# Kernel tuning notes

Hardware: AMD Instinct MI355X
Metric: run time of the kernel (lower is better)

Reference implementation:

```python
import jax, jax.numpy as jnp
import numpy as np

ITERS = 3
K = 64
C = 256


def setup_inputs() -> dict:
    key = jax.random.key(0)
    ks = jax.random.split(key, 6)
    N, H, W = 2, 60, 60
    cnn_feature = jax.random.normal(ks[0], (N, C, H, W), dtype=jnp.float32)
    points = jax.random.normal(ks[1], (N, 3, H, W), dtype=jnp.float32)
    # torch Linear params: weight (out, in), bias (out,)
    s1 = 1.0 / np.sqrt(C)
    s2 = 1.0 / np.sqrt(2 * C)
    mlp_w = jax.random.uniform(ks[2], (C, C), jnp.float32, -s1, s1)
    mlp_b = jax.random.uniform(ks[3], (C,), jnp.float32, -s1, s1)
    rnn_w = jax.random.uniform(ks[4], (C, 2 * C), jnp.float32, -s2, s2)
    rnn_b = jax.random.uniform(ks[5], (C,), jnp.float32, -s2, s2)
    return {"cnn_feature": cnn_feature, "points": points, "mlp_w": mlp_w,
            "mlp_b": mlp_b, "rnn_w": rnn_w, "rnn_b": rnn_b}


def reference(cnn_feature, points, mlp_w, mlp_b, rnn_w, rnn_b):
    N, Cc, H, W = cnn_feature.shape
    HW = H * W
    pts = points.reshape(N, 3, HW).transpose(0, 2, 1)  # (N, HW, 3)
    # pairwise Euclidean distances via Gram matrix
    r = jnp.einsum('nid,njd->nij', pts, pts)           # (N, HW, HW)
    sq = jnp.einsum('nid,nid->ni', pts, pts)           # (N, HW)
    D = jnp.sqrt(jnp.maximum(sq[:, :, None] + sq[:, None, :] - 2.0 * r, 0.0))
    _, idx = jax.lax.top_k(-D, K)                      # (N, HW, K) smallest distances

    h = cnn_feature.transpose(0, 2, 3, 1).reshape(N, HW, Cc)  # (N, HW, C)
    bidx = jnp.arange(N)[:, None, None]
    for _ in range(ITERS):
        nb = h[bidx, idx]                              # (N, HW, K, C) gather
        nb = jax.nn.relu(jnp.einsum('nskc,dc->nskd', nb, mlp_w) + mlp_b)
        message = nb.mean(axis=2)                      # (N, HW, C)
        nh = jnp.concatenate([h, message], axis=-1)    # (N, HW, 2C)
        h = jax.nn.relu(jnp.einsum('nsc,dc->nsd', nh, rnn_w) + rnn_b)
    h = h.reshape(N, H, W, Cc).transpose(0, 3, 1, 2)   # (N, C, H, W)
    return jnp.concatenate([cnn_feature, h], axis=1)   # (N, 2C, H, W)
```

## Files before the change

### kernel.cpp

```cpp
#include <hip/hip_runtime.h>
#include <stdint.h>

typedef unsigned int uint;

#define HW 3600
#define NBATCH 2
#define CDIM 256
#define KNN 64
#define M_REAL 7200
#define PADM 7232
#define QPB 8

using short8  = __attribute__((ext_vector_type(8))) short;
using floatx4 = __attribute__((ext_vector_type(4))) float;

__device__ inline unsigned short f2bf(float f) {
    uint u = __float_as_uint(f);
    uint r = u + 0x7FFFu + ((u >> 16) & 1u);
    return (unsigned short)(r >> 16);
}
__device__ inline float bf2f(unsigned short b) {
    return __uint_as_float(((uint)b) << 16);
}

__device__ inline void wave_select(uint* hist, uint* s_bin, uint* s_want,
                                   int lane, uint want) {
    uint h0 = hist[4 * lane + 0], h1 = hist[4 * lane + 1];
    uint h2 = hist[4 * lane + 2], h3 = hist[4 * lane + 3];
    hist[4 * lane + 0] = 0; hist[4 * lane + 1] = 0;
    hist[4 * lane + 2] = 0; hist[4 * lane + 3] = 0;
    uint c4 = h0 + h1 + h2 + h3;
    uint v = c4;
    #pragma unroll
    for (int off = 1; off < 64; off <<= 1) {
        uint o = __shfl_up(v, off, 64);
        if (lane >= off) v += o;
    }
    uint below = v - c4;
    if (below < want && want <= v) {
        uint b = 4 * lane, c = below;
        if (c + h0 < want) { c += h0; b = 4 * lane + 1;
            if (c + h1 < want) { c += h1; b = 4 * lane + 2;
                if (c + h2 < want) { c += h2; b = 4 * lane + 3; } } }
        *s_bin = b;
        *s_want = want - c;
    }
}

__global__ __launch_bounds__(512) void topk_kernel(const float* __restrict__ points,
                                                   int* __restrict__ idx_out) {
    const int wv = threadIdx.x >> 6;
    const int lane = threadIdx.x & 63;
    const int q = blockIdx.x * QPB + wv;
    const int n = (blockIdx.x * QPB) / HW;
    const int i = q - n * HW;

    __shared__ __align__(16) float sx[HW], sy[HW], sz[HW];
    __shared__ uint hist[QPB][256];
    __shared__ uint s_bin[QPB], s_want[QPB], s_cnt[QPB];

    const float* __restrict__ px = points + (size_t)n * 3 * HW;

    for (int j4 = threadIdx.x; j4 < HW / 4; j4 += 512) {
        *(float4*)&sx[j4 * 4] = ((const float4*)px)[j4];
        *(float4*)&sy[j4 * 4] = ((const float4*)px)[j4 + HW / 4];
        *(float4*)&sz[j4 * 4] = ((const float4*)px)[j4 + 2 * (HW / 4)];
    }
    hist[wv][4 * lane + 0] = 0; hist[wv][4 * lane + 1] = 0;
    hist[wv][4 * lane + 2] = 0; hist[wv][4 * lane + 3] = 0;
    if (lane == 0) s_cnt[wv] = 0;
    __syncthreads();

    const float xi = sx[i], yi = sy[i], zi = sz[i];
    const float sqi = xi * xi + yi * yi + zi * zi;

    uint qp[30];
    #pragma unroll
    for (int c = 0; c < 30; ++c) qp[c] = 0xFFFFFFFFu;
    #pragma unroll
    for (int c = 0; c < 15; ++c) {
        int j0 = (c << 8) + lane * 4;
        if (j0 < HW) {
            float4 x4 = *(const float4*)&sx[j0];
            float4 y4 = *(const float4*)&sy[j0];
            float4 z4 = *(const float4*)&sz[j0];
            float d0 = fmaxf(sqi + (x4.x * x4.x + y4.x * y4.x + z4.x * z4.x)
                             - 2.0f * (xi * x4.x + yi * y4.x + zi * z4.x), 0.0f);
            float d1 = fmaxf(sqi + (x4.y * x4.y + y4.y * y4.y + z4.y * z4.y)
                             - 2.0f * (xi * x4.y + yi * y4.y + zi * z4.y), 0.0f);
            float d2 = fmaxf(sqi + (x4.z * x4.z + y4.z * y4.z + z4.z * z4.z)
                             - 2.0f * (xi * x4.z + yi * y4.z + zi * z4.z), 0.0f);
            float d3 = fmaxf(sqi + (x4.w * x4.w + y4.w * y4.w + z4.w * z4.w)
                             - 2.0f * (xi * x4.w + yi * y4.w + zi * z4.w), 0.0f);
            uint k0 = (uint)fminf(d0 * 1024.0f, 65535.0f);
            uint k1 = (uint)fminf(d1 * 1024.0f, 65535.0f);
            uint k2 = (uint)fminf(d2 * 1024.0f, 65535.0f);
            uint k3 = (uint)fminf(d3 * 1024.0f, 65535.0f);
            qp[2 * c]     = k0 | (k1 << 16);
            qp[2 * c + 1] = k2 | (k3 << 16);
        }
    }
    #define Q16(c, t) ((qp[2 * (c) + ((t) >> 1)] >> (((t) & 1) << 4)) & 0xFFFFu)

    #pragma unroll
    for (int c = 0; c < 15; ++c)
        #pragma unroll
        for (int t = 0; t < 4; ++t) atomicAdd(&hist[wv][Q16(c, t) >> 8], 1u);
    __syncthreads();
    wave_select(&hist[wv][0], &s_bin[wv], &s_want[wv], lane, KNN);
    __syncthreads();
    const uint qT8 = s_bin[wv];
    const uint want2 = s_want[wv];
    __syncthreads();

    #pragma unroll
    for (int c = 0; c < 15; ++c)
        #pragma unroll
        for (int t = 0; t < 4; ++t) {
            uint k = Q16(c, t);
            if ((k >> 8) == qT8) atomicAdd(&hist[wv][k & 255u], 1u);
        }
    __syncthreads();
    wave_select(&hist[wv][0], &s_bin[wv], &s_want[wv], lane, want2);
    __syncthreads();
    const uint qT16 = (qT8 << 8) | s_bin[wv];
    const uint want3 = s_want[wv];

    #pragma unroll
    for (int c = 0; c < 15; ++c)
        #pragma unroll
        for (int t = 0; t < 4; ++t) {
            if (Q16(c, t) < qT16) {
                uint pos = atomicAdd(&s_cnt[wv], 1u);
                if (pos < KNN)
                    idx_out[(size_t)q * KNN + pos] = (c << 8) + lane * 4 + t;
            }
        }
    unsigned long long used = 0ULL;
    const int base = KNN - (int)want3;
    for (int r = 0; r < (int)want3; ++r) {
        unsigned long long best = ~0ULL;
        #pragma unroll
        for (int c = 0; c < 15; ++c) {
            int j0 = (c << 8) + lane * 4;
            if (j0 < HW) {
                float4 x4 = *(const float4*)&sx[j0];
                float4 y4 = *(const float4*)&sy[j0];
                float4 z4 = *(const float4*)&sz[j0];
                float dd[4];
                dd[0] = fmaxf(sqi + (x4.x * x4.x + y4.x * y4.x + z4.x * z4.x)
                              - 2.0f * (xi * x4.x + yi * y4.x + zi * z4.x), 0.0f);
                dd[1] = fmaxf(sqi + (x4.y * x4.y + y4.y * y4.y + z4.y * z4.y)
                              - 2.0f * (xi * x4.y + yi * y4.y + zi * z4.y), 0.0f);
                dd[2] = fmaxf(sqi + (x4.z * x4.z + y4.z * y4.z + z4.z * z4.z)
                              - 2.0f * (xi * x4.z + yi * y4.z + zi * z4.z), 0.0f);
                dd[3] = fmaxf(sqi + (x4.w * x4.w + y4.w * y4.w + z4.w * z4.w)
                              - 2.0f * (xi * x4.w + yi * y4.w + zi * z4.w), 0.0f);
                #pragma unroll
                for (int t = 0; t < 4; ++t) {
                    int slot = c * 4 + t;
                    if (Q16(c, t) == qT16 && !((used >> slot) & 1ULL)) {
                        unsigned long long key =
                            ((unsigned long long)__float_as_uint(dd[t]) << 32)
                            | (uint)(j0 + t);
                        if (key < best) best = key;
                    }
                }
            }
        }
        #pragma unroll
        for (int off = 1; off < 64; off <<= 1) {
            unsigned long long o = __shfl_xor(best, off, 64);
            if (o < best) best = o;
        }
        uint jw = (uint)best;
        if (lane == 0) idx_out[(size_t)q * KNN + base + r] = (int)jw;
        if ((int)((jw & 255u) >> 2) == lane)
            used |= 1ULL << (((jw >> 8) << 2) | (jw & 3u));
    }
    #undef Q16
}

__global__ __launch_bounds__(256) void setup_kernel(
    const float* __restrict__ mw, const float* __restrict__ rw,
    unsigned short* __restrict__ mo, unsigned short* __restrict__ ro) {
    int i = blockIdx.x * 256 + threadIdx.x;
    if (i < 65536) mo[i] = f2bf(mw[i]);
    ro[i] = f2bf(rw[i]);
}

__global__ __launch_bounds__(256) void init_h(const float* __restrict__ cnn,
                                              unsigned short* __restrict__ NH,
                                              float* __restrict__ out) {
    __shared__ float tile[32][33];
    const int hw0 = blockIdx.x * 32;
    const int c0 = blockIdx.y * 32;
    const int n = blockIdx.z;
    const int tx = threadIdx.x & 31;
    const int ty = threadIdx.x >> 5;
    const float* __restrict__ src = cnn + (size_t)n * CDIM * HW;
    #pragma unroll
    for (int r = 0; r < 4; ++r) {
        int cc = ty + r * 8;
        int hw = hw0 + tx;
        if (hw < HW) {
            float v = src[(size_t)(c0 + cc) * HW + hw];
            tile[cc][tx] = v;
            out[(size_t)n * (2 * CDIM * HW) + (size_t)(c0 + cc) * HW + hw] = v;
        }
    }
    __syncthreads();
    #pragma unroll
    for (int r = 0; r < 4; ++r) {
        int hh = ty + r * 8;
        int hw = hw0 + hh;
        if (hw < HW) NH[(size_t)(n * HW + hw) * 512 + c0 + tx] = f2bf(tile[tx][hh]);
    }
}

#define LDKP 264
__global__ __launch_bounds__(256) void gemm_mfma(
    const unsigned short* __restrict__ A, int lda,
    const unsigned short* __restrict__ W, int ldw,
    const float* __restrict__ bias,
    unsigned short* __restrict__ Cb, int ldc,
    float* __restrict__ outp, int mode, int Kk) {
    __shared__ __align__(16) unsigned short As[64 * LDKP];
    __shared__ __align__(16) unsigned short Bs[64 * LDKP];
    const int m0 = blockIdx.x * 64;
    const int n0 = blockIdx.y * 64;
    const int tid = threadIdx.x;
    const int lane = tid & 63;
    const int w = tid >> 6;
    const int wm = (w & 1) * 32;
    const int wn = (w >> 1) * 32;
    const int l15 = lane & 15;
    const int qd = lane >> 4;

    floatx4 acc[2][2];
    #pragma unroll
    for (int a = 0; a < 2; ++a)
        #pragma unroll
        for (int b = 0; b < 2; ++b)
            acc[a][b] = (floatx4){0.f, 0.f, 0.f, 0.f};

    const int srow = tid >> 5;
    const int scol = (tid & 31) * 8;

    for (int k0 = 0; k0 < Kk; k0 += 256) {
        if (k0) __syncthreads();
        #pragma unroll
        for (int r8 = 0; r8 < 8; ++r8) {
            int row = r8 * 8 + srow;
            *(float4*)&As[row * LDKP + scol] =
                *(const float4*)&A[(size_t)(m0 + row) * lda + k0 + scol];
            *(float4*)&Bs[row * LDKP + scol] =
                *(const float4*)&W[(size_t)(n0 + row) * ldw + k0 + scol];
        }
        __syncthreads();
        #pragma unroll
        for (int ks = 0; ks < 256; ks += 32) {
            short8 a0 = *(const short8*)&As[(wm + l15) * LDKP + ks + qd * 8];
            short8 a1 = *(const short8*)&As[(wm + 16 + l15) * LDKP + ks + qd * 8];
            short8 b0 = *(const short8*)&Bs[(wn + l15) * LDKP + ks + qd * 8];
            short8 b1 = *(const short8*)&Bs[(wn + 16 + l15) * LDKP + ks + qd * 8];
            acc[0][0] = __builtin_amdgcn_mfma_f32_16x16x32_bf16(a0, b0, acc[0][0], 0, 0, 0);
            acc[0][1] = __builtin_amdgcn_mfma_f32_16x16x32_bf16(a0, b1, acc[0][1], 0, 0, 0);
            acc[1][0] = __builtin_amdgcn_mfma_f32_16x16x32_bf16(a1, b0, acc[1][0], 0, 0, 0);
            acc[1][1] = __builtin_amdgcn_mfma_f32_16x16x32_bf16(a1, b1, acc[1][1], 0, 0, 0);
        }
    }

    #pragma unroll
    for (int in = 0; in < 2; ++in) {
        int col = n0 + wn + in * 16 + l15;
        float bv = bias[col];
        #pragma unroll
        for (int im = 0; im < 2; ++im) {
            int mb = m0 + wm + im * 16 + qd * 4;
            if (mode == 0) {
                #pragma unroll
                for (int r = 0; r < 4; ++r)
                    Cb[(size_t)(mb + r) * ldc + col] =
                        f2bf(fmaxf(acc[im][in][r] + bv, 0.0f));
            } else if (mb < M_REAL) {
                int nb = mb / HW;
                int hw = mb - nb * HW;
                float4 o;
                o.x = fmaxf(acc[im][in][0] + bv, 0.0f);
                o.y = fmaxf(acc[im][in][1] + bv, 0.0f);
                o.z = fmaxf(acc[im][in][2] + bv, 0.0f);
                o.w = fmaxf(acc[im][in][3] + bv, 0.0f);
                *(float4*)&outp[(size_t)nb * (2 * CDIM * HW)
                                + (size_t)(CDIM + col) * HW + hw] = o;
            }
        }
    }
}

__global__ __launch_bounds__(256) void gather_mean(const unsigned short* __restrict__ T,
                                                   const int* __restrict__ idx,
                                                   unsigned short* __restrict__ NH) {
    const int q = blockIdx.x * 4 + (threadIdx.x >> 6);
    const int lane = threadIdx.x & 63;
    const int n = q / HW;
    const int half = lane >> 5;
    const int c8 = (lane & 31) * 8;

    const int nbrL = idx[(size_t)q * KNN + lane];
    float acc[8] = {0, 0, 0, 0, 0, 0, 0, 0};
    #pragma unroll 4
    for (int it = 0; it < 32; ++it) {
        int k = 2 * it + half;
        int j = __shfl(nbrL, k, 64);
        j = min(max(j, 0), HW - 1);
        int r = n * HW + j;
        uint4 v = *(const uint4*)&T[(size_t)r * CDIM + c8];
        acc[0] += bf2f((unsigned short)(v.x & 0xFFFFu));
        acc[1] += bf2f((unsigned short)(v.x >> 16));
        acc[2] += bf2f((unsigned short)(v.y & 0xFFFFu));
        acc[3] += bf2f((unsigned short)(v.y >> 16));
        acc[4] += bf2f((unsigned short)(v.z & 0xFFFFu));
        acc[5] += bf2f((unsigned short)(v.z >> 16));
        acc[6] += bf2f((unsigned short)(v.w & 0xFFFFu));
        acc[7] += bf2f((unsigned short)(v.w >> 16));
    }
    #pragma unroll
    for (int c = 0; c < 8; ++c) acc[c] += __shfl_xor(acc[c], 32, 64);
    if (half == 0) {
        uint4 o;
        o.x = (uint)f2bf(acc[0] * (1.0f / KNN)) | ((uint)f2bf(acc[1] * (1.0f / KNN)) << 16);
        o.y = (uint)f2bf(acc[2] * (1.0f / KNN)) | ((uint)f2bf(acc[3] * (1.0f / KNN)) << 16);
        o.z = (uint)f2bf(acc[4] * (1.0f / KNN)) | ((uint)f2bf(acc[5] * (1.0f / KNN)) << 16);
        o.w = (uint)f2bf(acc[6] * (1.0f / KNN)) | ((uint)f2bf(acc[7] * (1.0f / KNN)) << 16);
        *(uint4*)&NH[(size_t)q * 512 + CDIM + c8] = o;
    }
}

extern "C" void kernel_launch(void* const* d_in, const int* in_sizes, int n_in,
                              void* d_out, int out_size, void* d_ws, size_t ws_size,
                              hipStream_t stream) {
    const float* cnn   = (const float*)d_in[0];
    const float* pts   = (const float*)d_in[1];
    const float* mlp_w = (const float*)d_in[2];
    const float* mlp_b = (const float*)d_in[3];
    const float* rnn_w = (const float*)d_in[4];
    const float* rnn_b = (const float*)d_in[5];
    float* out = (float*)d_out;

    unsigned short* NHa    = (unsigned short*)d_ws;
    unsigned short* NHb    = NHa + (size_t)PADM * 512;
    unsigned short* Tb     = NHb + (size_t)PADM * 512;
    unsigned short* mlpw_b = Tb + (size_t)PADM * CDIM;
    unsigned short* rnnw_b = mlpw_b + 65536;
    int*            idx    = (int*)(rnnw_b + 131072);

    setup_kernel<<<512, 256, 0, stream>>>(mlp_w, rnn_w, mlpw_b, rnnw_b);
    topk_kernel<<<M_REAL / QPB, 512, 0, stream>>>(pts, idx);
    init_h<<<dim3(113, 8, NBATCH), 256, 0, stream>>>(cnn, NHa, out);

    unsigned short* cur = NHa;
    unsigned short* nxt = NHb;
    for (int it = 0; it < 3; ++it) {
        gemm_mfma<<<dim3(PADM / 64, CDIM / 64), 256, 0, stream>>>(
            cur, 512, mlpw_b, CDIM, mlp_b, Tb, CDIM, nullptr, 0, CDIM);
        gather_mean<<<M_REAL / 4, 256, 0, stream>>>(Tb, idx, cur);
        if (it < 2) {
            gemm_mfma<<<dim3(PADM / 64, CDIM / 64), 256, 0, stream>>>(
                cur, 512, rnnw_b, 512, rnn_b, nxt, 512, nullptr, 0, 512);
            unsigned short* tmp = cur; cur = nxt; nxt = tmp;
        } else {
            gemm_mfma<<<dim3(PADM / 64, CDIM / 64), 256, 0, stream>>>(
                cur, 512, rnnw_b, 512, rnn_b, nullptr, 0, out, 1, 512);
        }
    }
}
```

Before: 243.3 us.

## Merge setup, top-k and init kernels into one launch; cache tie-bin candidates

The three independent prologue kernels (bf16 weight conversion, kNN top-k selection, feature transpose/init) become one heterogeneous kernel dispatched by block index, so they share a single launch and can run concurrently on the device. The top-k path changes its point layout to interleaved float4 with a strided per-lane assignment, and for the final tie bin it caches up to four candidate keys per lane in registers instead of recomputing all distances each selection round. A fallback keeps the old rescan loop when any lane holds more than four tie candidates. The shared-memory union sizes every block for the top-k footprint, which may limit occupancy of the lighter block types.

After: 206.9 us. 15.0% less time.

```diff
diff --git a/kernel.cpp b/kernel.cpp
--- a/kernel.cpp
+++ b/kernel.cpp
@@ -2,6 +2,7 @@
 #include <stdint.h>
 
 typedef unsigned int uint;
+typedef unsigned long long ull;
 
 #define HW 3600
 #define NBATCH 2
@@ -10,6 +11,10 @@
 #define M_REAL 7200
 #define PADM 7232
 #define QPB 8
+
+#define TKB 900
+#define IHB 904
+#define SUB 64
 
 using short8  = __attribute__((ext_vector_type(8))) short;
 using floatx4 = __attribute__((ext_vector_type(4))) float;
@@ -47,175 +52,200 @@
     }
 }
 
-__global__ __launch_bounds__(512) void topk_kernel(const float* __restrict__ points,
-                                                   int* __restrict__ idx_out) {
+union MegaSmem {
+    struct {
+        float4 pts[HW];
+        uint hist[QPB][256];
+        uint s_bin[QPB], s_want[QPB], s_cnt[QPB];
+    } tk;
+    struct { float tile[2][32][33]; } ih;
+};
+
+__global__ __launch_bounds__(512) void mega_kernel(
+    const float* __restrict__ points, int* __restrict__ idx_out,
+    const float* __restrict__ cnn, unsigned short* __restrict__ NH,
+    float* __restrict__ out,
+    const float* __restrict__ mw, const float* __restrict__ rw,
+    unsigned short* __restrict__ mo, unsigned short* __restrict__ ro) {
+    __shared__ MegaSmem sm;
+    const int blk = blockIdx.x;
+
+    if (blk >= TKB + IHB) {
+        int i0 = (blk - TKB - IHB) * 2048 + threadIdx.x * 4;
+        float4 v = *(const float4*)&rw[i0];
+        uint2 p;
+        p.x = (uint)f2bf(v.x) | ((uint)f2bf(v.y) << 16);
+        p.y = (uint)f2bf(v.z) | ((uint)f2bf(v.w) << 16);
+        *(uint2*)&ro[i0] = p;
+        if (i0 < 65536) {
+            float4 m = *(const float4*)&mw[i0];
+            p.x = (uint)f2bf(m.x) | ((uint)f2bf(m.y) << 16);
+            p.y = (uint)f2bf(m.z) | ((uint)f2bf(m.w) << 16);
+            *(uint2*)&mo[i0] = p;
+        }
+        return;
+    }
+
+    if (blk >= TKB) {
+        const int b = blk - TKB;
+        const int n = b / 452;
+        const int r = b - n * 452;
+        const int hw0 = (r % 113) * 32;
+        const int c0 = (r / 113) * 64 + ((threadIdx.x >> 8) << 5);
+        const int t8 = threadIdx.x & 255;
+        const int tx = t8 & 31;
+        const int ty = t8 >> 5;
+        float (*tile)[33] = sm.ih.tile[threadIdx.x >> 8];
+        const float* __restrict__ src = cnn + (size_t)n * CDIM * HW;
+        #pragma unroll
+        for (int rr = 0; rr < 4; ++rr) {
+            int cc = ty + rr * 8;
+            int hw = hw0 + tx;
+            if (hw < HW) {
+                float v = src[(size_t)(c0 + cc) * HW + hw];
+                tile[cc][tx] = v;
+                out[(size_t)n * (2 * CDIM * HW) + (size_t)(c0 + cc) * HW + hw] = v;
+            }
+        }
+        __syncthreads();
+        #pragma unroll
+        for (int rr = 0; rr < 4; ++rr) {
+            int hh = ty + rr * 8;
+            int hw = hw0 + hh;
+            if (hw < HW)
+                NH[(size_t)(n * HW + hw) * 512 + c0 + tx] = f2bf(tile[tx][hh]);
+        }
+        return;
+    }
+
     const int wv = threadIdx.x >> 6;
     const int lane = threadIdx.x & 63;
-    const int q = blockIdx.x * QPB + wv;
-    const int n = (blockIdx.x * QPB) / HW;
+    const int q = blk * QPB + wv;
+    const int n = (blk * QPB) / HW;
     const int i = q - n * HW;
 
-    __shared__ __align__(16) float sx[HW], sy[HW], sz[HW];
-    __shared__ uint hist[QPB][256];
-    __shared__ uint s_bin[QPB], s_want[QPB], s_cnt[QPB];
-
     const float* __restrict__ px = points + (size_t)n * 3 * HW;
-
-    for (int j4 = threadIdx.x; j4 < HW / 4; j4 += 512) {
-        *(float4*)&sx[j4 * 4] = ((const float4*)px)[j4];
-        *(float4*)&sy[j4 * 4] = ((const float4*)px)[j4 + HW / 4];
-        *(float4*)&sz[j4 * 4] = ((const float4*)px)[j4 + 2 * (HW / 4)];
-    }
-    hist[wv][4 * lane + 0] = 0; hist[wv][4 * lane + 1] = 0;
-    hist[wv][4 * lane + 2] = 0; hist[wv][4 * lane + 3] = 0;
-    if (lane == 0) s_cnt[wv] = 0;
-    __syncthreads();
-
-    const float xi = sx[i], yi = sy[i], zi = sz[i];
+    const float* __restrict__ py = px + HW;
+    const float* __restrict__ pz = py + HW;
+
+    for (int j = threadIdx.x; j < HW; j += 512)
+        sm.tk.pts[j] = make_float4(px[j], py[j], pz[j], 0.0f);
+    sm.tk.hist[wv][4 * lane + 0] = 0; sm.tk.hist[wv][4 * lane + 1] = 0;
+    sm.tk.hist[wv][4 * lane + 2] = 0; sm.tk.hist[wv][4 * lane + 3] = 0;
+    if (lane == 0) sm.tk.s_cnt[wv] = 0;
+    __syncthreads();
+
+    float4 pq = sm.tk.pts[i];
+    const float xi = pq.x, yi = pq.y, zi = pq.z;
     const float sqi = xi * xi + yi * yi + zi * zi;
 
-    uint qp[30];
-    #pragma unroll
-    for (int c = 0; c < 30; ++c) qp[c] = 0xFFFFFFFFu;
-    #pragma unroll
-    for (int c = 0; c < 15; ++c) {
-        int j0 = (c << 8) + lane * 4;
-        if (j0 < HW) {
-            float4 x4 = *(const float4*)&sx[j0];
-            float4 y4 = *(const float4*)&sy[j0];
-            float4 z4 = *(const float4*)&sz[j0];
-            float d0 = fmaxf(sqi + (x4.x * x4.x + y4.x * y4.x + z4.x * z4.x)
-                             - 2.0f * (xi * x4.x + yi * y4.x + zi * z4.x), 0.0f);
-            float d1 = fmaxf(sqi + (x4.y * x4.y + y4.y * y4.y + z4.y * z4.y)
-                             - 2.0f * (xi * x4.y + yi * y4.y + zi * z4.y), 0.0f);
-            float d2 = fmaxf(sqi + (x4.z * x4.z + y4.z * y4.z + z4.z * z4.z)
-                             - 2.0f * (xi * x4.z + yi * y4.z + zi * z4.z), 0.0f);
-            float d3 = fmaxf(sqi + (x4.w * x4.w + y4.w * y4.w + z4.w * z4.w)
-                             - 2.0f * (xi * x4.w + yi * y4.w + zi * z4.w), 0.0f);
-            uint k0 = (uint)fminf(d0 * 1024.0f, 65535.0f);
-            uint k1 = (uint)fminf(d1 * 1024.0f, 65535.0f);
-            uint k2 = (uint)fminf(d2 * 1024.0f, 65535.0f);
-            uint k3 = (uint)fminf(d3 * 1024.0f, 65535.0f);
-            qp[2 * c]     = k0 | (k1 << 16);
-            qp[2 * c + 1] = k2 | (k3 << 16);
-        }
-    }
-    #define Q16(c, t) ((qp[2 * (c) + ((t) >> 1)] >> (((t) & 1) << 4)) & 0xFFFFu)
-
-    #pragma unroll
-    for (int c = 0; c < 15; ++c)
-        #pragma unroll
-        for (int t = 0; t < 4; ++t) atomicAdd(&hist[wv][Q16(c, t) >> 8], 1u);
-    __syncthreads();
-    wave_select(&hist[wv][0], &s_bin[wv], &s_want[wv], lane, KNN);
-    __syncthreads();
-    const uint qT8 = s_bin[wv];
-    const uint want2 = s_want[wv];
-    __syncthreads();
-
-    #pragma unroll
-    for (int c = 0; c < 15; ++c)
-        #pragma unroll
-        for (int t = 0; t < 4; ++t) {
-            uint k = Q16(c, t);
-            if ((k >> 8) == qT8) atomicAdd(&hist[wv][k & 255u], 1u);
-        }
-    __syncthreads();
-    wave_select(&hist[wv][0], &s_bin[wv], &s_want[wv], lane, want2);
-    __syncthreads();
-    const uint qT16 = (qT8 << 8) | s_bin[wv];
-    const uint want3 = s_want[wv];
-
-    #pragma unroll
-    for (int c = 0; c < 15; ++c)
-        #pragma unroll
-        for (int t = 0; t < 4; ++t) {
-            if (Q16(c, t) < qT16) {
-                uint pos = atomicAdd(&s_cnt[wv], 1u);
-                if (pos < KNN)
-                    idx_out[(size_t)q * KNN + pos] = (c << 8) + lane * 4 + t;
+    uint qp[29];
+    #pragma unroll
+    for (int s = 0; s < 57; ++s) {
+        int j = (s << 6) + lane;
+        uint q16 = 0xFFFFu;
+        if (j < HW) {
+            float4 p = sm.tk.pts[j];
+            float d2 = fmaxf(sqi + (p.x * p.x + p.y * p.y + p.z * p.z)
+                             - 2.0f * (xi * p.x + yi * p.y + zi * p.z), 0.0f);
+            q16 = (uint)fminf(d2 * 1024.0f, 65535.0f);
+        }
+        if (s & 1) qp[s >> 1] |= q16 << 16; else qp[s >> 1] = q16;
+    }
+    #define Q16(s) ((qp[(s) >> 1] >> (((s) & 1) << 4)) & 0xFFFFu)
+
+    #pragma unroll
+    for (int s = 0; s < 57; ++s) {
+        int j = (s << 6) + lane;
+        if (j < HW) atomicAdd(&sm.tk.hist[wv][Q16(s) >> 8], 1u);
+    }
+    __syncthreads();
+    wave_select(&sm.tk.hist[wv][0], &sm.tk.s_bin[wv], &sm.tk.s_want[wv], lane, KNN);
+    __syncthreads();
+    const uint qT8 = sm.tk.s_bin[wv];
+    const uint want2 = sm.tk.s_want[wv];
+    __syncthreads();
+
+    #pragma unroll
+    for (int s = 0; s < 57; ++s) {
+        int j = (s << 6) + lane;
+        uint k = Q16(s);
+        if (j < HW && (k >> 8) == qT8)
+            atomicAdd(&sm.tk.hist[wv][k & 255u], 1u);
+    }
+    __syncthreads();
+    wave_select(&sm.tk.hist[wv][0], &sm.tk.s_bin[wv], &sm.tk.s_want[wv], lane, want2);
+    __syncthreads();
+    const uint qT16 = (qT8 << 8) | sm.tk.s_bin[wv];
+    const uint want3 = sm.tk.s_want[wv];
+
+    #pragma unroll
+    for (int s = 0; s < 57; ++s) {
+        if (Q16(s) < qT16) {
+            uint pos = atomicAdd(&sm.tk.s_cnt[wv], 1u);
+            if (pos < KNN) idx_out[(size_t)q * KNN + pos] = (s << 6) + lane;
+        }
+    }
+
+    ull cand[4] = {~0ULL, ~0ULL, ~0ULL, ~0ULL};
+    int ncand = 0;
+    #pragma unroll
+    for (int s = 0; s < 57; ++s) {
+        int j = (s << 6) + lane;
+        if (j < HW && Q16(s) == qT16) {
+            float4 p = sm.tk.pts[j];
+            float d2 = fmaxf(sqi + (p.x * p.x + p.y * p.y + p.z * p.z)
+                             - 2.0f * (xi * p.x + yi * p.y + zi * p.z), 0.0f);
+            ull key = ((ull)__float_as_uint(d2) << 32) | (uint)j;
+            if      (ncand == 0) cand[0] = key;
+            else if (ncand == 1) cand[1] = key;
+            else if (ncand == 2) cand[2] = key;
+            else if (ncand == 3) cand[3] = key;
+            ++ncand;
+        }
+    }
+    const int base = KNN - (int)want3;
+    if (__ballot(ncand > 4) == 0ULL) {
+        for (int r = 0; r < (int)want3; ++r) {
+            ull best = cand[0] < cand[1] ? cand[0] : cand[1];
+            ull b23  = cand[2] < cand[3] ? cand[2] : cand[3];
+            best = best < b23 ? best : b23;
+            #pragma unroll
+            for (int off = 1; off < 64; off <<= 1) {
+                ull o = __shfl_xor(best, off, 64);
+                if (o < best) best = o;
             }
-        }
-    unsigned long long used = 0ULL;
-    const int base = KNN - (int)want3;
-    for (int r = 0; r < (int)want3; ++r) {
-        unsigned long long best = ~0ULL;
-        #pragma unroll
-        for (int c = 0; c < 15; ++c) {
-            int j0 = (c << 8) + lane * 4;
-            if (j0 < HW) {
-                float4 x4 = *(const float4*)&sx[j0];
-                float4 y4 = *(const float4*)&sy[j0];
-                float4 z4 = *(const float4*)&sz[j0];
-                float dd[4];
-                dd[0] = fmaxf(sqi + (x4.x * x4.x + y4.x * y4.x + z4.x * z4.x)
-                              - 2.0f * (xi * x4.x + yi * y4.x + zi * z4.x), 0.0f);
-                dd[1] = fmaxf(sqi + (x4.y * x4.y + y4.y * y4.y + z4.y * z4.y)
-                              - 2.0f * (xi * x4.y + yi * y4.y + zi * z4.y), 0.0f);
-                dd[2] = fmaxf(sqi + (x4.z * x4.z + y4.z * y4.z + z4.z * z4.z)
-                              - 2.0f * (xi * x4.z + yi * y4.z + zi * z4.z), 0.0f);
-                dd[3] = fmaxf(sqi + (x4.w * x4.w + y4.w * y4.w + z4.w * z4.w)
-                              - 2.0f * (xi * x4.w + yi * y4.w + zi * z4.w), 0.0f);
-                #pragma unroll
-                for (int t = 0; t < 4; ++t) {
-                    int slot = c * 4 + t;
-                    if (Q16(c, t) == qT16 && !((used >> slot) & 1ULL)) {
-                        unsigned long long key =
-                            ((unsigned long long)__float_as_uint(dd[t]) << 32)
-                            | (uint)(j0 + t);
-                        if (key < best) best = key;
-                    }
+            if (lane == 0) idx_out[(size_t)q * KNN + base + r] = (int)(uint)best;
+            #pragma unroll
+            for (int c = 0; c < 4; ++c)
+                if (cand[c] == best) cand[c] = ~0ULL;
+        }
+    } else {
+        ull used = 0ULL;
+        for (int r = 0; r < (int)want3; ++r) {
+            ull best = ~0ULL;
+            #pragma unroll
+            for (int s = 0; s < 57; ++s) {
+                int j = (s << 6) + lane;
+                if (j < HW && Q16(s) == qT16 && !((used >> s) & 1ULL)) {
+                    float4 p = sm.tk.pts[j];
+                    float d2 = fmaxf(sqi + (p.x * p.x + p.y * p.y + p.z * p.z)
+                                     - 2.0f * (xi * p.x + yi * p.y + zi * p.z), 0.0f);
+                    ull key = ((ull)__float_as_uint(d2) << 32) | (uint)j;
+                    if (key < best) best = key;
                 }
             }
-        }
-        #pragma unroll
-        for (int off = 1; off < 64; off <<= 1) {
-            unsigned long long o = __shfl_xor(best, off, 64);
-            if (o < best) best = o;
-        }
-        uint jw = (uint)best;
-        if (lane == 0) idx_out[(size_t)q * KNN + base + r] = (int)jw;
-        if ((int)((jw & 255u) >> 2) == lane)
-            used |= 1ULL << (((jw >> 8) << 2) | (jw & 3u));
+            #pragma unroll
+            for (int off = 1; off < 64; off <<= 1) {
+                ull o = __shfl_xor(best, off, 64);
+                if (o < best) best = o;
+            }
+            uint jw = (uint)best;
+            if (lane == 0) idx_out[(size_t)q * KNN + base + r] = (int)jw;
+            if ((int)(jw & 63u) == lane) used |= 1ULL << (jw >> 6);
+        }
     }
     #undef Q16
-}
-
-__global__ __launch_bounds__(256) void setup_kernel(
-    const float* __restrict__ mw, const float* __restrict__ rw,
-    unsigned short* __restrict__ mo, unsigned short* __restrict__ ro) {
-    int i = blockIdx.x * 256 + threadIdx.x;
-    if (i < 65536) mo[i] = f2bf(mw[i]);
-    ro[i] = f2bf(rw[i]);
-}
-
-__global__ __launch_bounds__(256) void init_h(const float* __restrict__ cnn,
-                                              unsigned short* __restrict__ NH,
-                                              float* __restrict__ out) {
-    __shared__ float tile[32][33];
-    const int hw0 = blockIdx.x * 32;
-    const int c0 = blockIdx.y * 32;
-    const int n = blockIdx.z;
-    const int tx = threadIdx.x & 31;
-    const int ty = threadIdx.x >> 5;
-    const float* __restrict__ src = cnn + (size_t)n * CDIM * HW;
-    #pragma unroll
-    for (int r = 0; r < 4; ++r) {
-        int cc = ty + r * 8;
-        int hw = hw0 + tx;
-        if (hw < HW) {
-            float v = src[(size_t)(c0 + cc) * HW + hw];
-            tile[cc][tx] = v;
-            out[(size_t)n * (2 * CDIM * HW) + (size_t)(c0 + cc) * HW + hw] = v;
-        }
-    }
-    __syncthreads();
-    #pragma unroll
-    for (int r = 0; r < 4; ++r) {
-        int hh = ty + r * 8;
-        int hw = hw0 + hh;
-        if (hw < HW) NH[(size_t)(n * HW + hw) * 512 + c0 + tx] = f2bf(tile[tx][hh]);
-    }
 }
 
 #define LDKP 264
@@ -355,9 +385,8 @@
     unsigned short* rnnw_b = mlpw_b + 65536;
     int*            idx    = (int*)(rnnw_b + 131072);
 
-    setup_kernel<<<512, 256, 0, stream>>>(mlp_w, rnn_w, mlpw_b, rnnw_b);
-    topk_kernel<<<M_REAL / QPB, 512, 0, stream>>>(pts, idx);
-    init_h<<<dim3(113, 8, NBATCH), 256, 0, stream>>>(cnn, NHa, out);
+    mega_kernel<<<TKB + IHB + SUB, 512, 0, stream>>>(
+        pts, idx, cnn, NHa, out, mlp_w, rnn_w, mlpw_b, rnnw_b);
 
     unsigned short* cur = NHa;
     unsigned short* nxt = NHb;
```
